# Optimization experiments

Hardware: AMD Instinct MI355X
Metric: run time of the kernel (lower is better)

Reference implementation:

```python
import jax, jax.numpy as jnp
import numpy as np

N_EMBED = 1024
NUM_HEADS = 16
HEAD_DIM = N_EMBED // NUM_HEADS

def setup_inputs() -> dict:
    key = jax.random.key(0)
    ks = jax.random.split(key, 7)
    s = 0.02
    return {
        "x": jax.random.normal(ks[0], (2, 2048, N_EMBED), dtype=jnp.float32),
        "Wqkv": jax.random.normal(ks[1], (N_EMBED, 3 * N_EMBED), dtype=jnp.float32) * s,
        "bqkv": jax.random.normal(ks[2], (3 * N_EMBED,), dtype=jnp.float32) * s,
        "W1": jax.random.normal(ks[3], (N_EMBED, 4 * N_EMBED), dtype=jnp.float32) * s,
        "b1": jax.random.normal(ks[4], (4 * N_EMBED,), dtype=jnp.float32) * s,
        "W2": jax.random.normal(ks[5], (4 * N_EMBED, N_EMBED), dtype=jnp.float32) * s,
        "b2": jax.random.normal(ks[6], (N_EMBED,), dtype=jnp.float32) * s,
    }

def reference(x, Wqkv, bqkv, W1, b1, W2, b2):
    B, T, N = x.shape
    h, n = NUM_HEADS, HEAD_DIM
    # LayerNorm in source is identity; dropout=0 (eval)
    qkv = x @ Wqkv + bqkv  # [B,T,3N]
    q, k, v = jnp.split(qkv, 3, axis=-1)
    q = q.reshape(B, T, h, n).transpose(0, 2, 1, 3)  # [B,h,T,n]
    k = k.reshape(B, T, h, n).transpose(0, 2, 1, 3)
    v = v.reshape(B, T, h, n).transpose(0, 2, 1, 3)
    scores = jnp.einsum('bhqd,bhkd->bhqk', q, k) / jnp.sqrt(jnp.float32(n))
    causal = jnp.tril(jnp.ones((T, T), dtype=bool))
    scores = jnp.where(causal, scores, -jnp.inf)
    attn = jax.nn.softmax(scores, axis=-1)
    out = jnp.einsum('bhqk,bhkd->bhqd', attn, v)
    out = out.transpose(0, 2, 1, 3).reshape(B, T, N)
    x = x + out  # residual (no output projection in source)
    # MLP
    hcore = jax.nn.relu(x @ W1 + b1)
    x = x + (hcore @ W2 + b2)
    return x
```

## Files before the change

### kernel.cpp

```cpp
#include <hip/hip_runtime.h>

#define NEMB 1024
#define NH 16
#define HD 64
#define TT 2048
#define BTOT 4096

typedef unsigned short u16;
typedef __bf16 bf16_t;
typedef bf16_t bf16x8 __attribute__((ext_vector_type(8)));
typedef float f32x4 __attribute__((ext_vector_type(4)));
typedef u16 u16x4 __attribute__((ext_vector_type(4)));

typedef const __attribute__((address_space(1))) void* gvp;
typedef __attribute__((address_space(3))) void* lvp;

static __device__ __forceinline__ u16 f2bf(float f) {
  unsigned u = __builtin_bit_cast(unsigned, f);
  u += 0x7fffu + ((u >> 16) & 1u);
  return (u16)(u >> 16);
}

__global__ void cvt_bf16_k(const float* __restrict__ in, u16* __restrict__ out, int n4) {
  int i = blockIdx.x * blockDim.x + threadIdx.x;
  if (i >= n4) return;
  float4 f = ((const float4*)in)[i];
  u16x4 o = { f2bf(f.x), f2bf(f.y), f2bf(f.z), f2bf(f.w) };
  ((u16x4*)out)[i] = o;
}

__global__ void transpose_cvt_k(const float* __restrict__ in, u16* __restrict__ out, int R, int C) {
  __shared__ float tile[32][33];
  int bx = blockIdx.x, by = blockIdx.y;
  int tx = threadIdx.x, ty = threadIdx.y;
  #pragma unroll
  for (int j = 0; j < 32; j += 8)
    tile[ty + j][tx] = in[(size_t)(by * 32 + ty + j) * C + bx * 32 + tx];
  __syncthreads();
  #pragma unroll
  for (int j = 0; j < 32; j += 8)
    out[(size_t)(bx * 32 + ty + j) * R + by * 32 + tx] = f2bf(tile[tx][ty + j]);
}

template<int EPI>
__global__ void gemm_bt(const u16* __restrict__ A, const u16* __restrict__ Bt,
                        const float* __restrict__ bias, int M, int N, int K,
                        const float* __restrict__ res, float* __restrict__ outf,
                        u16* __restrict__ o0, u16* __restrict__ o1, u16* __restrict__ o2)
{
  __shared__ u16 As[128 * 32];
  __shared__ u16 Bs[128 * 32];
  const int tid = threadIdx.x;
  const int wave = tid >> 6, lane = tid & 63;
  const int l16 = lane & 15, lq = lane >> 4;
  const int row0 = blockIdx.x * 128, col0 = blockIdx.y * 128;
  const int wm = (wave >> 1) * 64, wn = (wave & 1) * 64;
  f32x4 acc[4][4] = {};

  for (int k0 = 0; k0 < K; k0 += 32) {
    #pragma unroll
    for (int c = 0; c < 2; ++c) {
      int li = c * 256 + wave * 64 + lane;
      const u16* ga = A  + (size_t)(row0 + (li >> 2)) * K + k0 + (li & 3) * 8;
      const u16* gb = Bt + (size_t)(col0 + (li >> 2)) * K + k0 + (li & 3) * 8;
      __builtin_amdgcn_global_load_lds((gvp)ga, (lvp)&As[(c * 256 + wave * 64) * 8], 16, 0, 0);
      __builtin_amdgcn_global_load_lds((gvp)gb, (lvp)&Bs[(c * 256 + wave * 64) * 8], 16, 0, 0);
    }
    __syncthreads();
    bf16x8 af[4], bfr[4];
    #pragma unroll
    for (int i = 0; i < 4; ++i) af[i]  = *(const bf16x8*)&As[(wm + i * 16 + l16) * 32 + lq * 8];
    #pragma unroll
    for (int j = 0; j < 4; ++j) bfr[j] = *(const bf16x8*)&Bs[(wn + j * 16 + l16) * 32 + lq * 8];
    #pragma unroll
    for (int i = 0; i < 4; ++i)
      #pragma unroll
      for (int j = 0; j < 4; ++j)
        acc[i][j] = __builtin_amdgcn_mfma_f32_16x16x32_bf16(af[i], bfr[j], acc[i][j], 0, 0, 0);
    __syncthreads();
  }

  #pragma unroll
  for (int i = 0; i < 4; ++i)
    #pragma unroll
    for (int j = 0; j < 4; ++j)
      #pragma unroll
      for (int r = 0; r < 4; ++r) {
        int grow = row0 + wm + i * 16 + lq * 4 + r;
        int gcol = col0 + wn + j * 16 + l16;
        float v = acc[i][j][r] + bias[gcol];
        if constexpr (EPI == 0) {
          int b = grow >> 11, t = grow & 2047;
          int sec = gcol >> 10, rem = gcol & 1023;
          int h = rem >> 6, d = rem & 63;
          u16 bits = f2bf(v);
          size_t bh = (size_t)(b * NH + h);
          if (sec == 0)      o0[(bh * TT + t) * HD + d] = bits;
          else if (sec == 1) o1[(bh * TT + t) * HD + d] = bits;
          else               o2[(bh * HD + d) * TT + t] = bits;
        } else if constexpr (EPI == 1) {
          v = fmaxf(v, 0.f);
          o0[(size_t)grow * N + gcol] = f2bf(v);
        } else {
          size_t idx = (size_t)grow * N + gcol;
          outf[idx] = v + res[idx];
        }
      }
}

__global__ void attn_k(const u16* __restrict__ qb, const u16* __restrict__ kb,
                       const u16* __restrict__ vtb, const float* __restrict__ x,
                       float* __restrict__ xres, u16* __restrict__ xresbf)
{
  __shared__ u16 P[4][32 * 72];
  const int bh = blockIdx.y;
  const int b = bh >> 4, h = bh & 15;
  const int tid = threadIdx.x, wave = tid >> 6, lane = tid & 63;
  const int l16 = lane & 15, lq = lane >> 4;
  const u16* qh = qb + (size_t)bh * TT * HD;
  const u16* kh = kb + (size_t)bh * TT * HD;
  const u16* vh = vtb + (size_t)bh * HD * TT;
  const int q0 = blockIdx.x * 128 + wave * 32;

  bf16x8 qf[2][2];
  #pragma unroll
  for (int m = 0; m < 2; ++m)
    #pragma unroll
    for (int kd = 0; kd < 2; ++kd)
      qf[m][kd] = *(const bf16x8*)&qh[(q0 + m * 16 + l16) * HD + kd * 32 + lq * 8];

  f32x4 oacc[2][4] = {};
  float mrow[2][4], lrow[2][4];
  #pragma unroll
  for (int m = 0; m < 2; ++m)
    #pragma unroll
    for (int r = 0; r < 4; ++r) { mrow[m][r] = -1e30f; lrow[m][r] = 0.f; }

  const int nkv = (q0 + 31) / 64 + 1;
  u16* Pw = P[wave];

  for (int kv = 0; kv < nkv; ++kv) {
    const int kv0 = kv * 64;
    const bool diag = (kv0 + 63 > q0);
    f32x4 sacc[2][4] = {};
    #pragma unroll
    for (int n = 0; n < 4; ++n)
      #pragma unroll
      for (int kd = 0; kd < 2; ++kd) {
        bf16x8 kf = *(const bf16x8*)&kh[(kv0 + n * 16 + l16) * HD + kd * 32 + lq * 8];
        #pragma unroll
        for (int m = 0; m < 2; ++m)
          sacc[m][n] = __builtin_amdgcn_mfma_f32_16x16x32_bf16(qf[m][kd], kf, sacc[m][n], 0, 0, 0);
      }

    #pragma unroll
    for (int m = 0; m < 2; ++m)
      #pragma unroll
      for (int r = 0; r < 4; ++r) {
        const int qr = q0 + m * 16 + lq * 4 + r;
        float rmax = -1e30f;
        #pragma unroll
        for (int n = 0; n < 4; ++n) {
          float s = sacc[m][n][r] * 0.125f;
          if (diag && (kv0 + n * 16 + l16) > qr) s = -1e30f;
          sacc[m][n][r] = s;
          rmax = fmaxf(rmax, s);
        }
        #pragma unroll
        for (int off = 1; off < 16; off <<= 1)
          rmax = fmaxf(rmax, __shfl_xor(rmax, off, 64));
        const float mold = mrow[m][r];
        const float mnew = fmaxf(mold, rmax);
        const float scl = __expf(mold - mnew);
        float rsum = 0.f;
        #pragma unroll
        for (int n = 0; n < 4; ++n) {
          float p = __expf(sacc[m][n][r] - mnew);
          sacc[m][n][r] = p;
          rsum += p;
        }
        #pragma unroll
        for (int off = 1; off < 16; off <<= 1)
          rsum += __shfl_xor(rsum, off, 64);
        mrow[m][r] = mnew;
        lrow[m][r] = lrow[m][r] * scl + rsum;
        #pragma unroll
        for (int nd = 0; nd < 4; ++nd) oacc[m][nd][r] *= scl;
      }

    #pragma unroll
    for (int m = 0; m < 2; ++m)
      #pragma unroll
      for (int n = 0; n < 4; ++n)
        #pragma unroll
        for (int r = 0; r < 4; ++r)
          Pw[(m * 16 + lq * 4 + r) * 72 + n * 16 + l16] = f2bf(sacc[m][n][r]);

    #pragma unroll
    for (int kk = 0; kk < 2; ++kk) {
      bf16x8 pf[2];
      #pragma unroll
      for (int m = 0; m < 2; ++m)
        pf[m] = *(const bf16x8*)&Pw[(m * 16 + l16) * 72 + kk * 32 + lq * 8];
      #pragma unroll
      for (int nd = 0; nd < 4; ++nd) {
        bf16x8 vf = *(const bf16x8*)&vh[(nd * 16 + l16) * TT + kv0 + kk * 32 + lq * 8];
        #pragma unroll
        for (int m = 0; m < 2; ++m)
          oacc[m][nd] = __builtin_amdgcn_mfma_f32_16x16x32_bf16(pf[m], vf, oacc[m][nd], 0, 0, 0);
      }
    }
  }

  #pragma unroll
  for (int m = 0; m < 2; ++m)
    #pragma unroll
    for (int r = 0; r < 4; ++r) {
      const float inv = 1.f / lrow[m][r];
      const int t = q0 + m * 16 + lq * 4 + r;
      const size_t rowbase = ((size_t)b * TT + t) * NEMB + h * HD;
      #pragma unroll
      for (int nd = 0; nd < 4; ++nd) {
        size_t idx = rowbase + nd * 16 + l16;
        float v = oacc[m][nd][r] * inv + x[idx];
        xres[idx] = v;
        xresbf[idx] = f2bf(v);
      }
    }
}

extern "C" void kernel_launch(void* const* d_in, const int* in_sizes, int n_in,
                              void* d_out, int out_size, void* d_ws, size_t ws_size,
                              hipStream_t stream) {
  const float* x    = (const float*)d_in[0];
  const float* Wqkv = (const float*)d_in[1];
  const float* bqkv = (const float*)d_in[2];
  const float* W1   = (const float*)d_in[3];
  const float* b1   = (const float*)d_in[4];
  const float* W2   = (const float*)d_in[5];
  const float* b2   = (const float*)d_in[6];
  float* out = (float*)d_out;

  char* ws = (char*)d_ws;
  u16* x_bf   = (u16*)(ws);
  u16* wqkvt  = (u16*)(ws + 8388608);
  u16* w1t    = (u16*)(ws + 14680064);
  u16* w2t    = (u16*)(ws + 23068672);
  u16* qbuf   = (u16*)(ws + 31457280);
  u16* kbuf   = (u16*)(ws + 39845888);
  u16* vtbuf  = (u16*)(ws + 48234496);
  float* xres = (float*)(ws + 56623104);
  u16* xresbf = (u16*)(ws + 73400320);
  u16* hbuf   = (u16*)(ws + 81788928);

  cvt_bf16_k<<<4096, 256, 0, stream>>>(x, x_bf, 1048576);
  transpose_cvt_k<<<dim3(96, 32),  dim3(32, 8), 0, stream>>>(Wqkv, wqkvt, 1024, 3072);
  transpose_cvt_k<<<dim3(128, 32), dim3(32, 8), 0, stream>>>(W1, w1t, 1024, 4096);
  transpose_cvt_k<<<dim3(32, 128), dim3(32, 8), 0, stream>>>(W2, w2t, 4096, 1024);

  gemm_bt<0><<<dim3(32, 24), 256, 0, stream>>>(x_bf, wqkvt, bqkv, BTOT, 3 * NEMB, NEMB,
                                               nullptr, nullptr, qbuf, kbuf, vtbuf);
  attn_k<<<dim3(16, 32), 256, 0, stream>>>(qbuf, kbuf, vtbuf, x, xres, xresbf);
  gemm_bt<1><<<dim3(32, 32), 256, 0, stream>>>(xresbf, w1t, b1, BTOT, 4 * NEMB, NEMB,
                                               nullptr, nullptr, hbuf, nullptr, nullptr);
  gemm_bt<2><<<dim3(32, 8), 256, 0, stream>>>(hbuf, w2t, b2, BTOT, NEMB, 4 * NEMB,
                                              xres, out, nullptr, nullptr, nullptr);
}
```

Measured before the change: 464.1 us.

## Shrink attention tiles to 16 rows per wave with XCD-aware, heavy-first block order

The attention kernel now gives each wave 16 query rows instead of 32 and launches 1024 blocks, with a 1D grid remapped so each XCD handles a contiguous group of heads. Blocks are issued longest causal row first to balance load. K and V fragments are loaded into registers before they are used, and launch bounds request higher occupancy. This aims to raise parallelism and hide memory latency, at the cost of loading each K/V tile once per 16 rows instead of once per 32.

Result: slower. 493.1 us (+6.3%).

```diff
diff --git a/kernel.cpp b/kernel.cpp
--- a/kernel.cpp
+++ b/kernel.cpp
@@ -108,125 +108,126 @@
       }
 }
 
-__global__ void attn_k(const u16* __restrict__ qb, const u16* __restrict__ kb,
-                       const u16* __restrict__ vtb, const float* __restrict__ x,
-                       float* __restrict__ xres, u16* __restrict__ xresbf)
+__global__ void __launch_bounds__(256, 4)
+attn_k(const u16* __restrict__ qb, const u16* __restrict__ kb,
+       const u16* __restrict__ vtb, const float* __restrict__ x,
+       float* __restrict__ xres, u16* __restrict__ xresbf)
 {
-  __shared__ u16 P[4][32 * 72];
-  const int bh = blockIdx.y;
+  __shared__ u16 P[4][16 * 72];
+  const int id = blockIdx.x;
+  const int xcd = id & 7, r8 = id >> 3;
+  const int bh = xcd * 4 + (r8 >> 5);
+  const int xq = 31 - (r8 & 31);
   const int b = bh >> 4, h = bh & 15;
   const int tid = threadIdx.x, wave = tid >> 6, lane = tid & 63;
   const int l16 = lane & 15, lq = lane >> 4;
   const u16* qh = qb + (size_t)bh * TT * HD;
   const u16* kh = kb + (size_t)bh * TT * HD;
   const u16* vh = vtb + (size_t)bh * HD * TT;
-  const int q0 = blockIdx.x * 128 + wave * 32;
-
-  bf16x8 qf[2][2];
-  #pragma unroll
-  for (int m = 0; m < 2; ++m)
-    #pragma unroll
-    for (int kd = 0; kd < 2; ++kd)
-      qf[m][kd] = *(const bf16x8*)&qh[(q0 + m * 16 + l16) * HD + kd * 32 + lq * 8];
-
-  f32x4 oacc[2][4] = {};
-  float mrow[2][4], lrow[2][4];
-  #pragma unroll
-  for (int m = 0; m < 2; ++m)
-    #pragma unroll
-    for (int r = 0; r < 4; ++r) { mrow[m][r] = -1e30f; lrow[m][r] = 0.f; }
-
-  const int nkv = (q0 + 31) / 64 + 1;
+  const int q0 = (xq * 4 + wave) * 16;
+
+  bf16x8 qf[2];
+  #pragma unroll
+  for (int kd = 0; kd < 2; ++kd)
+    qf[kd] = *(const bf16x8*)&qh[(q0 + l16) * HD + kd * 32 + lq * 8];
+
+  f32x4 oacc[4] = {};
+  float mrow[4], lrow[4];
+  #pragma unroll
+  for (int r = 0; r < 4; ++r) { mrow[r] = -1e30f; lrow[r] = 0.f; }
+
+  const int nkv = (q0 >> 6) + 1;
   u16* Pw = P[wave];
 
   for (int kv = 0; kv < nkv; ++kv) {
     const int kv0 = kv * 64;
     const bool diag = (kv0 + 63 > q0);
-    f32x4 sacc[2][4] = {};
+
+    bf16x8 kf[8];
     #pragma unroll
     for (int n = 0; n < 4; ++n)
       #pragma unroll
-      for (int kd = 0; kd < 2; ++kd) {
-        bf16x8 kf = *(const bf16x8*)&kh[(kv0 + n * 16 + l16) * HD + kd * 32 + lq * 8];
-        #pragma unroll
-        for (int m = 0; m < 2; ++m)
-          sacc[m][n] = __builtin_amdgcn_mfma_f32_16x16x32_bf16(qf[m][kd], kf, sacc[m][n], 0, 0, 0);
+      for (int kd = 0; kd < 2; ++kd)
+        kf[n * 2 + kd] = *(const bf16x8*)&kh[(kv0 + n * 16 + l16) * HD + kd * 32 + lq * 8];
+    f32x4 sacc[4] = {};
+    #pragma unroll
+    for (int n = 0; n < 4; ++n)
+      #pragma unroll
+      for (int kd = 0; kd < 2; ++kd)
+        sacc[n] = __builtin_amdgcn_mfma_f32_16x16x32_bf16(qf[kd], kf[n * 2 + kd], sacc[n], 0, 0, 0);
+
+    bf16x8 vf0[4];
+    #pragma unroll
+    for (int nd = 0; nd < 4; ++nd)
+      vf0[nd] = *(const bf16x8*)&vh[(nd * 16 + l16) * TT + kv0 + lq * 8];
+
+    #pragma unroll
+    for (int r = 0; r < 4; ++r) {
+      const int qr = q0 + lq * 4 + r;
+      float rmax = -1e30f;
+      #pragma unroll
+      for (int n = 0; n < 4; ++n) {
+        float s = sacc[n][r] * 0.125f;
+        if (diag && (kv0 + n * 16 + l16) > qr) s = -1e30f;
+        sacc[n][r] = s;
+        rmax = fmaxf(rmax, s);
       }
-
-    #pragma unroll
-    for (int m = 0; m < 2; ++m)
-      #pragma unroll
-      for (int r = 0; r < 4; ++r) {
-        const int qr = q0 + m * 16 + lq * 4 + r;
-        float rmax = -1e30f;
-        #pragma unroll
-        for (int n = 0; n < 4; ++n) {
-          float s = sacc[m][n][r] * 0.125f;
-          if (diag && (kv0 + n * 16 + l16) > qr) s = -1e30f;
-          sacc[m][n][r] = s;
-          rmax = fmaxf(rmax, s);
-        }
-        #pragma unroll
-        for (int off = 1; off < 16; off <<= 1)
-          rmax = fmaxf(rmax, __shfl_xor(rmax, off, 64));
-        const float mold = mrow[m][r];
-        const float mnew = fmaxf(mold, rmax);
-        const float scl = __expf(mold - mnew);
-        float rsum = 0.f;
-        #pragma unroll
-        for (int n = 0; n < 4; ++n) {
-          float p = __expf(sacc[m][n][r] - mnew);
-          sacc[m][n][r] = p;
-          rsum += p;
-        }
-        #pragma unroll
-        for (int off = 1; off < 16; off <<= 1)
-          rsum += __shfl_xor(rsum, off, 64);
-        mrow[m][r] = mnew;
-        lrow[m][r] = lrow[m][r] * scl + rsum;
-        #pragma unroll
-        for (int nd = 0; nd < 4; ++nd) oacc[m][nd][r] *= scl;
+      #pragma unroll
+      for (int off = 1; off < 16; off <<= 1)
+        rmax = fmaxf(rmax, __shfl_xor(rmax, off, 64));
+      const float mold = mrow[r];
+      const float mnew = fmaxf(mold, rmax);
+      const float scl = __expf(mold - mnew);
+      float rsum = 0.f;
+      #pragma unroll
+      for (int n = 0; n < 4; ++n) {
+        float p = __expf(sacc[n][r] - mnew);
+        sacc[n][r] = p;
+        rsum += p;
       }
-
-    #pragma unroll
-    for (int m = 0; m < 2; ++m)
-      #pragma unroll
-      for (int n = 0; n < 4; ++n)
-        #pragma unroll
-        for (int r = 0; r < 4; ++r)
-          Pw[(m * 16 + lq * 4 + r) * 72 + n * 16 + l16] = f2bf(sacc[m][n][r]);
-
-    #pragma unroll
-    for (int kk = 0; kk < 2; ++kk) {
-      bf16x8 pf[2];
-      #pragma unroll
-      for (int m = 0; m < 2; ++m)
-        pf[m] = *(const bf16x8*)&Pw[(m * 16 + l16) * 72 + kk * 32 + lq * 8];
-      #pragma unroll
-      for (int nd = 0; nd < 4; ++nd) {
-        bf16x8 vf = *(const bf16x8*)&vh[(nd * 16 + l16) * TT + kv0 + kk * 32 + lq * 8];
-        #pragma unroll
-        for (int m = 0; m < 2; ++m)
-          oacc[m][nd] = __builtin_amdgcn_mfma_f32_16x16x32_bf16(pf[m], vf, oacc[m][nd], 0, 0, 0);
-      }
+      #pragma unroll
+      for (int off = 1; off < 16; off <<= 1)
+        rsum += __shfl_xor(rsum, off, 64);
+      mrow[r] = mnew;
+      lrow[r] = lrow[r] * scl + rsum;
+      #pragma unroll
+      for (int nd = 0; nd < 4; ++nd) oacc[nd][r] *= scl;
+    }
+
+    #pragma unroll
+    for (int n = 0; n < 4; ++n)
+      #pragma unroll
+      for (int r = 0; r < 4; ++r)
+        Pw[(lq * 4 + r) * 72 + n * 16 + l16] = f2bf(sacc[n][r]);
+
+    bf16x8 vf1[4];
+    #pragma unroll
+    for (int nd = 0; nd < 4; ++nd)
+      vf1[nd] = *(const bf16x8*)&vh[(nd * 16 + l16) * TT + kv0 + 32 + lq * 8];
+
+    bf16x8 pf0 = *(const bf16x8*)&Pw[l16 * 72 + lq * 8];
+    #pragma unroll
+    for (int nd = 0; nd < 4; ++nd)
+      oacc[nd] = __builtin_amdgcn_mfma_f32_16x16x32_bf16(pf0, vf0[nd], oacc[nd], 0, 0, 0);
+    bf16x8 pf1 = *(const bf16x8*)&Pw[l16 * 72 + 32 + lq * 8];
+    #pragma unroll
+    for (int nd = 0; nd < 4; ++nd)
+      oacc[nd] = __builtin_amdgcn_mfma_f32_16x16x32_bf16(pf1, vf1[nd], oacc[nd], 0, 0, 0);
+  }
+
+  #pragma unroll
+  for (int r = 0; r < 4; ++r) {
+    const float inv = 1.f / lrow[r];
+    const int t = q0 + lq * 4 + r;
+    const size_t rowbase = ((size_t)b * TT + t) * NEMB + h * HD;
+    #pragma unroll
+    for (int nd = 0; nd < 4; ++nd) {
+      size_t idx = rowbase + nd * 16 + l16;
+      float v = oacc[nd][r] * inv + x[idx];
+      xres[idx] = v;
+      xresbf[idx] = f2bf(v);
     }
   }
-
-  #pragma unroll
-  for (int m = 0; m < 2; ++m)
-    #pragma unroll
-    for (int r = 0; r < 4; ++r) {
-      const float inv = 1.f / lrow[m][r];
-      const int t = q0 + m * 16 + lq * 4 + r;
-      const size_t rowbase = ((size_t)b * TT + t) * NEMB + h * HD;
-      #pragma unroll
-      for (int nd = 0; nd < 4; ++nd) {
-        size_t idx = rowbase + nd * 16 + l16;
-        float v = oacc[m][nd][r] * inv + x[idx];
-        xres[idx] = v;
-        xresbf[idx] = f2bf(v);
-      }
-    }
 }
 
 extern "C" void kernel_launch(void* const* d_in, const int* in_sizes, int n_in,
@@ -260,7 +261,7 @@
 
   gemm_bt<0><<<dim3(32, 24), 256, 0, stream>>>(x_bf, wqkvt, bqkv, BTOT, 3 * NEMB, NEMB,
                                                nullptr, nullptr, qbuf, kbuf, vtbuf);
-  attn_k<<<dim3(16, 32), 256, 0, stream>>>(qbuf, kbuf, vtbuf, x, xres, xresbf);
+  attn_k<<<1024, 256, 0, stream>>>(qbuf, kbuf, vtbuf, x, xres, xresbf);
   gemm_bt<1><<<dim3(32, 32), 256, 0, stream>>>(xresbf, w1t, b1, BTOT, 4 * NEMB, NEMB,
                                                nullptr, nullptr, hbuf, nullptr, nullptr);
   gemm_bt<2><<<dim3(32, 8), 256, 0, stream>>>(hbuf, w2t, b2, BTOT, NEMB, 4 * NEMB,
```
